# Kernel optimization log

Hardware: AMD Instinct MI355X
Metric: run time of the kernel (lower is better)

## Reference

```python
import jax, jax.numpy as jnp
import numpy as np

N_NODES = 100000
N_EDGES = 1600000
D_FEAT = 128
HIDDEN = 128
N_CLASSES = 10
NUM_GRAPHS = 64


def setup_inputs() -> dict:
    key = jax.random.key(0)
    ks = jax.random.split(key, 12)
    x = jax.random.normal(ks[0], (N_NODES, D_FEAT), dtype=jnp.float32)
    edge_index = jax.random.randint(ks[1], (2, N_EDGES), 0, N_NODES, dtype=jnp.int32)
    batch = jnp.sort(jax.random.randint(ks[2], (N_NODES,), 0, NUM_GRAPHS, dtype=jnp.int32))
    s = 1.0 / np.sqrt(HIDDEN)
    def lin(k, out_d, in_d):
        return jax.random.uniform(k, (out_d, in_d), jnp.float32, -s, s)
    return {
        "x": x,
        "edge_index": edge_index,
        "batch": batch,
        "W1l": lin(ks[3], HIDDEN, D_FEAT), "b1": jnp.zeros((HIDDEN,), jnp.float32),
        "W1r": lin(ks[4], HIDDEN, D_FEAT),
        "W2l": lin(ks[5], HIDDEN, HIDDEN), "b2": jnp.zeros((HIDDEN,), jnp.float32),
        "W2r": lin(ks[6], HIDDEN, HIDDEN),
        "W3l": lin(ks[7], HIDDEN, HIDDEN), "b3": jnp.zeros((HIDDEN,), jnp.float32),
        "W3r": lin(ks[8], HIDDEN, HIDDEN),
        "Wout": lin(ks[9], N_CLASSES, HIDDEN), "bout": jnp.zeros((N_CLASSES,), jnp.float32),
    }


def reference(x, edge_index, batch, W1l, b1, W1r, W2l, b2, W2r, W3l, b3, W3r, Wout, bout):
    src, dst = edge_index[0], edge_index[1]
    n = x.shape[0]

    def sage(h, Wl, b, Wr):
        # sum-aggregate neighbor features: scatter-add x[src] into dst rows
        agg = jax.ops.segment_sum(h[src], dst, num_segments=n)  # [N, d]
        return agg @ Wl.T + b + h @ Wr.T

    h = jax.nn.relu(sage(x, W1l, b1, W1r))
    h = jax.nn.relu(sage(h, W2l, b2, W2r))
    h = sage(h, W3l, b3, W3r)
    pooled = jax.ops.segment_sum(h, batch, num_segments=NUM_GRAPHS)  # [G, hidden]
    # dropout is identity in eval mode
    return pooled @ Wout.T + bout
```

## Files before the change

kernel.cpp:

```cpp
#include <hip/hip_runtime.h>
#include <hip/hip_bf16.h>

#define N_NODES  100000
#define N_EDGES  1600000
#define D_FEAT   128
#define HIDDEN   128
#define N_CLASSES 10
#define NUM_GRAPHS 64

#define NBUCK 250
#define NPB   400
#define BCAP  7168
#define GT    64
#define NPAD  100096
#define NTILES (NPAD / GT)

typedef __bf16 bf16x8 __attribute__((ext_vector_type(8)));
typedef float  f32x4  __attribute__((ext_vector_type(4)));

static __device__ __forceinline__ unsigned short f2bf(float f) {
    __bf16 b = (__bf16)f;
    return __builtin_bit_cast(unsigned short, b);
}

__global__ void conv_w6_kernel(const float* __restrict__ W0, const float* __restrict__ W1,
                               const float* __restrict__ W2, const float* __restrict__ W3,
                               const float* __restrict__ W4, const float* __restrict__ W5,
                               __bf16* __restrict__ out) {
    const float* Ws[6] = {W0, W1, W2, W3, W4, W5};
    int m = blockIdx.x >> 6;
    int i = (blockIdx.x & 63) * 256 + threadIdx.x;
    out[m * (HIDDEN * D_FEAT) + i] = (__bf16)Ws[m][i];
}

__global__ __launch_bounds__(256) void xconv_kernel(const float* __restrict__ x,
                                                    __bf16* __restrict__ out) {
    int i = blockIdx.x * 256 + threadIdx.x;
    bf16x8 o;
    if (i < N_NODES * 128 / 8) {
        float4 v0 = ((const float4*)x)[i * 2];
        float4 v1 = ((const float4*)x)[i * 2 + 1];
        o[0] = (__bf16)v0.x; o[1] = (__bf16)v0.y; o[2] = (__bf16)v0.z; o[3] = (__bf16)v0.w;
        o[4] = (__bf16)v1.x; o[5] = (__bf16)v1.y; o[6] = (__bf16)v1.z; o[7] = (__bf16)v1.w;
    } else {
        #pragma unroll
        for (int k = 0; k < 8; k++) o[k] = (__bf16)0.f;
    }
    if (i < NPAD * 128 / 8) ((bf16x8*)out)[i] = o;
}

__global__ __launch_bounds__(256) void bucket_scatter_kernel(const int* __restrict__ ei,
                                                             int* __restrict__ gcur,
                                                             int* __restrict__ bkt) {
    __shared__ int h[NBUCK];
    __shared__ int lb[NBUCK];
    int t = threadIdx.x;
    const int CH = N_EDGES / 256;
    for (int i = t; i < NBUCK; i += 256) h[i] = 0;
    __syncthreads();
    int e0 = blockIdx.x * CH;
    for (int e = e0 + t; e < e0 + CH; e += 256) {
        int d = ei[N_EDGES + e];
        atomicAdd(&h[d / NPB], 1);
    }
    __syncthreads();
    for (int i = t; i < NBUCK; i += 256) {
        lb[i] = atomicAdd(&gcur[i], h[i]);
        h[i] = 0;
    }
    __syncthreads();
    for (int e = e0 + t; e < e0 + CH; e += 256) {
        int s = ei[e];
        int d = ei[N_EDGES + e];
        int bb = d / NPB;
        int pos = lb[bb] + atomicAdd(&h[bb], 1);
        if (pos < BCAP) bkt[(size_t)bb * BCAP + pos] = ((d - bb * NPB) << 17) | s;
    }
}

__global__ __launch_bounds__(256) void bucket_csr_kernel(const int* __restrict__ bkt,
                                                         const int* __restrict__ gcur,
                                                         int2* __restrict__ rpse,
                                                         int* __restrict__ csr_src) {
    const int b = blockIdx.x;
    const int n0 = b * NPB;
    const int base = b * BCAP;
    int m = gcur[b]; if (m > BCAP) m = BCAP;
    __shared__ int cnt[NPB];
    __shared__ int part[128];
    __shared__ int excl[NPB];
    int t = threadIdx.x;
    for (int i = t; i < NPB; i += 256) cnt[i] = 0;
    __syncthreads();
    for (int e = t; e < m; e += 256) {
        int p = bkt[base + e];
        atomicAdd(&cnt[p >> 17], 1);
    }
    __syncthreads();
    int gs = 0;
    if (t < 100) { gs = cnt[4 * t] + cnt[4 * t + 1] + cnt[4 * t + 2] + cnt[4 * t + 3]; part[t] = gs; }
    else if (t < 128) part[t] = 0;
    __syncthreads();
    for (int off = 1; off < 128; off <<= 1) {
        int x = 0;
        if (t < 128 && t >= off) x = part[t - off];
        __syncthreads();
        if (t < 128) part[t] += x;
        __syncthreads();
    }
    if (t < 100) part[t] -= gs;
    __syncthreads();
    for (int i = t; i < NPB; i += 256) {
        int g = i >> 2;
        int e0 = part[g];
        for (int j = g * 4; j < i; j++) e0 += cnt[j];
        excl[i] = e0;
    }
    __syncthreads();
    for (int i = t; i < NPB; i += 256) {
        rpse[n0 + i] = make_int2(base + excl[i], base + excl[i] + cnt[i]);
    }
    __syncthreads();
    for (int i = t; i < NPB; i += 256) cnt[i] = excl[i];
    __syncthreads();
    for (int e = t; e < m; e += 256) {
        int p = bkt[base + e];
        int pos = base + atomicAdd(&cnt[p >> 17], 1);
        csr_src[pos] = p & 0x1FFFF;
    }
}

__global__ __launch_bounds__(256) void gather_kernel(
    const __bf16* __restrict__ h, const int2* __restrict__ rpse,
    const int* __restrict__ csr_src, __bf16* __restrict__ agg, int N)
{
    int nid = blockIdx.x * 16 + (threadIdx.x >> 4);
    if (nid >= N) return;
    int f8 = threadIdx.x & 15;
    int2 se = rpse[nid];

    float a[8] = {0.f, 0.f, 0.f, 0.f, 0.f, 0.f, 0.f, 0.f};

    int j = se.x;
    for (; j + 3 < se.y; j += 4) {
        int s0 = csr_src[j];
        int s1 = csr_src[j + 1];
        int s2 = csr_src[j + 2];
        int s3 = csr_src[j + 3];
        bf16x8 u0 = ((const bf16x8*)h)[(size_t)s0 * 16 + f8];
        bf16x8 u1 = ((const bf16x8*)h)[(size_t)s1 * 16 + f8];
        bf16x8 u2 = ((const bf16x8*)h)[(size_t)s2 * 16 + f8];
        bf16x8 u3 = ((const bf16x8*)h)[(size_t)s3 * 16 + f8];
        #pragma unroll
        for (int i = 0; i < 8; i++)
            a[i] += ((float)u0[i] + (float)u1[i]) + ((float)u2[i] + (float)u3[i]);
    }
    for (; j < se.y; j++) {
        int s0 = csr_src[j];
        bf16x8 u0 = ((const bf16x8*)h)[(size_t)s0 * 16 + f8];
        #pragma unroll
        for (int i = 0; i < 8; i++) a[i] += (float)u0[i];
    }
    bf16x8 o;
    #pragma unroll
    for (int i = 0; i < 8; i++) o[i] = (__bf16)a[i];
    ((bf16x8*)agg)[(size_t)nid * 16 + f8] = o;
}

template<bool RELU, bool POOL>
__global__ __launch_bounds__(256) void gemm_kernel(
    const __bf16* __restrict__ hA,
    const __bf16* __restrict__ hG,
    const __bf16* __restrict__ Wl, const __bf16* __restrict__ Wr,
    const float* __restrict__ bias,
    __bf16* __restrict__ outp, int M,
    const int* __restrict__ batch, float* __restrict__ pooled)
{
    const int tid  = threadIdx.x;
    const int wave = tid >> 6;
    const int lane = tid & 63;
    const int kq = lane >> 4;
    const int ln = lane & 15;
    const int node_base = blockIdx.x * GT;
    const int f_base = wave * 32;

    bf16x8 wfragL[2][4], wfragR[2][4];
    #pragma unroll
    for (int t = 0; t < 2; t++) {
        int wrow = f_base + t * 16 + ln;
        #pragma unroll
        for (int kc = 0; kc < 4; kc++) {
            int k0 = kc * 32 + kq * 8;
            wfragL[t][kc] = *(const bf16x8*)(Wl + wrow * 128 + k0);
            wfragR[t][kc] = *(const bf16x8*)(Wr + wrow * 128 + k0);
        }
    }
    float4 bias4[2];
    bias4[0] = *(const float4*)(bias + f_base + kq * 4);
    bias4[1] = *(const float4*)(bias + f_base + 16 + kq * 4);

    #pragma unroll 1
    for (int tau = 0; tau < GT / 16; tau++) {
        const int node = node_base + tau * 16 + ln;
        const size_t rowoff = (size_t)node * 128;
        bf16x8 gfrag[4], afrag[4];
        #pragma unroll
        for (int kc = 0; kc < 4; kc++) {
            gfrag[kc] = *(const bf16x8*)(hG + rowoff + kc * 32 + kq * 8);
            afrag[kc] = *(const bf16x8*)(hA + rowoff + kc * 32 + kq * 8);
        }

        f32x4 acc[2] = {(f32x4)(0.f), (f32x4)(0.f)};
        #pragma unroll
        for (int kc = 0; kc < 4; kc++) {
            #pragma unroll
            for (int t = 0; t < 2; t++) {
                acc[t] = __builtin_amdgcn_mfma_f32_16x16x32_bf16(wfragL[t][kc], gfrag[kc], acc[t], 0, 0, 0);
                acc[t] = __builtin_amdgcn_mfma_f32_16x16x32_bf16(wfragR[t][kc], afrag[kc], acc[t], 0, 0, 0);
            }
        }

        if (!POOL) {
            if (node < M) {
                #pragma unroll
                for (int t = 0; t < 2; t++) {
                    int fc = f_base + t * 16 + kq * 4;
                    float v0 = acc[t][0] + bias4[t].x;
                    float v1 = acc[t][1] + bias4[t].y;
                    float v2 = acc[t][2] + bias4[t].z;
                    float v3 = acc[t][3] + bias4[t].w;
                    if (RELU) {
                        v0 = fmaxf(v0, 0.f); v1 = fmaxf(v1, 0.f);
                        v2 = fmaxf(v2, 0.f); v3 = fmaxf(v3, 0.f);
                    }
                    ushort4 o;
                    o.x = f2bf(v0); o.y = f2bf(v1); o.z = f2bf(v2); o.w = f2bf(v3);
                    *(ushort4*)(outp + rowoff + fc) = o;
                }
            }
        } else {
            const int n0 = node_base + tau * 16;
            const bool uni = (n0 + 15 < M) && (batch[n0] == batch[n0 + 15]);
            #pragma unroll
            for (int t = 0; t < 2; t++) {
                int fc = f_base + t * 16 + kq * 4;
                float v0 = acc[t][0] + bias4[t].x;
                float v1 = acc[t][1] + bias4[t].y;
                float v2 = acc[t][2] + bias4[t].z;
                float v3 = acc[t][3] + bias4[t].w;
                if (uni) {
                    #pragma unroll
                    for (int m = 1; m < 16; m <<= 1) {
                        v0 += __shfl_xor(v0, m);
                        v1 += __shfl_xor(v1, m);
                        v2 += __shfl_xor(v2, m);
                        v3 += __shfl_xor(v3, m);
                    }
                    if (ln == 0) {
                        float* p = &pooled[(size_t)batch[n0] * HIDDEN + fc];
                        unsafeAtomicAdd(p + 0, v0);
                        unsafeAtomicAdd(p + 1, v1);
                        unsafeAtomicAdd(p + 2, v2);
                        unsafeAtomicAdd(p + 3, v3);
                    }
                } else if (node < M) {
                    float* p = &pooled[(size_t)batch[node] * HIDDEN + fc];
                    unsafeAtomicAdd(p + 0, v0);
                    unsafeAtomicAdd(p + 1, v1);
                    unsafeAtomicAdd(p + 2, v2);
                    unsafeAtomicAdd(p + 3, v3);
                }
            }
        }
    }
}

__global__ void final_gemm_kernel(
    const float* __restrict__ pooled, const float* __restrict__ Wout,
    const float* __restrict__ bout, float* __restrict__ out)
{
    int idx = blockIdx.x * 64 + threadIdx.x;
    if (idx < NUM_GRAPHS * N_CLASSES) {
        int g = idx / N_CLASSES;
        int c = idx % N_CLASSES;
        float acc = bout[c];
        for (int k = 0; k < HIDDEN; k++)
            acc += pooled[g * HIDDEN + k] * Wout[c * HIDDEN + k];
        out[idx] = acc;
    }
}

extern "C" void kernel_launch(void* const* d_in, const int* in_sizes, int n_in,
                              void* d_out, int out_size, void* d_ws, size_t ws_size,
                              hipStream_t stream) {
    const float* x     = (const float*)d_in[0];
    const int*   ei    = (const int*)d_in[1];
    const int*   batch = (const int*)d_in[2];
    const float* W1l = (const float*)d_in[3];
    const float* b1  = (const float*)d_in[4];
    const float* W1r = (const float*)d_in[5];
    const float* W2l = (const float*)d_in[6];
    const float* b2  = (const float*)d_in[7];
    const float* W2r = (const float*)d_in[8];
    const float* W3l = (const float*)d_in[9];
    const float* b3  = (const float*)d_in[10];
    const float* W3r = (const float*)d_in[11];
    const float* Wout = (const float*)d_in[12];
    const float* bout = (const float*)d_in[13];
    float* out = (float*)d_out;

    char* ws = (char*)d_ws;
    size_t off = 0;
    const size_t NB = (size_t)NPAD * 128 * sizeof(__bf16);
    __bf16* B0    = (__bf16*)(ws + off); off += NB;
    __bf16* B1    = (__bf16*)(ws + off); off += NB;
    __bf16* B2    = (__bf16*)(ws + off); off += NB;
    float* pooled = (float*)(ws + off);  off += (size_t)NUM_GRAPHS * HIDDEN * sizeof(float);
    __bf16* wbf   = (__bf16*)(ws + off); off += 6 * (size_t)HIDDEN * D_FEAT * sizeof(__bf16);
    int2* rpse    = (int2*)(ws + off);   off += (size_t)N_NODES * sizeof(int2);
    int* csr_src  = (int*)(ws + off);    off += (size_t)NBUCK * BCAP * sizeof(int);
    int* bkt      = (int*)(ws + off);    off += (size_t)NBUCK * BCAP * sizeof(int);
    int* gcur     = (int*)(ws + off);    off += (NBUCK + 8) * sizeof(int);

    const int WSZ = HIDDEN * D_FEAT;

    conv_w6_kernel<<<6 * 64, 256, 0, stream>>>(W1l, W1r, W2l, W2r, W3l, W3r, wbf);
    xconv_kernel<<<NPAD * 128 / (256 * 8), 256, 0, stream>>>(x, B0);

    hipMemsetAsync(gcur, 0, NBUCK * sizeof(int), stream);
    hipMemsetAsync(pooled, 0, (size_t)NUM_GRAPHS * HIDDEN * sizeof(float), stream);
    bucket_scatter_kernel<<<256, 256, 0, stream>>>(ei, gcur, bkt);
    bucket_csr_kernel<<<NBUCK, 256, 0, stream>>>(bkt, gcur, rpse, csr_src);

    const int gath_grid = (N_NODES + 15) / 16;

    gather_kernel<<<gath_grid, 256, 0, stream>>>(B0, rpse, csr_src, B1, N_NODES);
    gemm_kernel<true, false><<<NTILES, 256, 0, stream>>>(
        B0, B1, wbf + 0 * WSZ, wbf + 1 * WSZ, b1, B2, N_NODES, nullptr, nullptr);

    gather_kernel<<<gath_grid, 256, 0, stream>>>(B2, rpse, csr_src, B1, N_NODES);
    gemm_kernel<true, false><<<NTILES, 256, 0, stream>>>(
        B2, B1, wbf + 2 * WSZ, wbf + 3 * WSZ, b2, B0, N_NODES, nullptr, nullptr);

    gather_kernel<<<gath_grid, 256, 0, stream>>>(B0, rpse, csr_src, B1, N_NODES);
    gemm_kernel<false, true><<<NTILES, 256, 0, stream>>>(
        B0, B1, wbf + 4 * WSZ, wbf + 5 * WSZ, b3, nullptr, N_NODES, batch, pooled);

    final_gemm_kernel<<<10, 64, 0, stream>>>(pooled, Wout, bout, out);
}
```

Before: 507.5 us.

## Sort CSR neighbor lists and stage GEMM input tiles into LDS asynchronously

Adds a per-node insertion-sort pass over each node's CSR source list (up to 48 entries) so gathers visit source rows in ascending order, aiming at better cache locality. The GEMM kernel now bulk-loads its 64-row input tiles of both operands into swizzled LDS with global_load_lds before computing, instead of per-lane global fragment loads. The sort adds an extra kernel with heavy LDS use and thread divergence. The ReLU added in the pooled branch only runs in the non-ReLU instantiation's dead path.

```diff
diff --git a/kernel.cpp b/kernel.cpp
--- a/kernel.cpp
+++ b/kernel.cpp
@@ -14,6 +14,7 @@
 #define GT    64
 #define NPAD  100096
 #define NTILES (NPAD / GT)
+#define SORT_CAP 48
 
 typedef __bf16 bf16x8 __attribute__((ext_vector_type(8)));
 typedef float  f32x4  __attribute__((ext_vector_type(4)));
@@ -21,6 +22,12 @@
 static __device__ __forceinline__ unsigned short f2bf(float f) {
     __bf16 b = (__bf16)f;
     return __builtin_bit_cast(unsigned short, b);
+}
+
+static __device__ __forceinline__ void async_copy16(void* lds, const void* g) {
+    __builtin_amdgcn_global_load_lds(
+        (const __attribute__((address_space(1))) void*)g,
+        (__attribute__((address_space(3))) void*)lds, 16, 0, 0);
 }
 
 __global__ void conv_w6_kernel(const float* __restrict__ W0, const float* __restrict__ W1,
@@ -130,6 +137,26 @@
     }
 }
 
+__global__ __launch_bounds__(256) void sort_csr_kernel(const int2* __restrict__ rpse,
+                                                       int* __restrict__ csr_src, int N) {
+    __shared__ int buf[SORT_CAP][256];
+    int nid = blockIdx.x * 256 + threadIdx.x;
+    if (nid >= N) return;
+    int t = threadIdx.x;
+    int2 se = rpse[nid];
+    int deg = se.y - se.x;
+    if (deg <= 1) return;
+    if (deg > SORT_CAP) deg = SORT_CAP;
+    for (int j = 0; j < deg; j++) buf[j][t] = csr_src[se.x + j];
+    for (int i = 1; i < deg; i++) {
+        int key = buf[i][t];
+        int j = i - 1;
+        while (j >= 0 && buf[j][t] > key) { buf[j + 1][t] = buf[j][t]; j--; }
+        buf[j + 1][t] = key;
+    }
+    for (int j = 0; j < deg; j++) csr_src[se.x + j] = buf[j][t];
+}
+
 __global__ __launch_bounds__(256) void gather_kernel(
     const __bf16* __restrict__ h, const int2* __restrict__ rpse,
     const int* __restrict__ csr_src, __bf16* __restrict__ agg, int N)
@@ -168,7 +195,7 @@
 }
 
 template<bool RELU, bool POOL>
-__global__ __launch_bounds__(256) void gemm_kernel(
+__global__ __launch_bounds__(256) void fused_gemm_kernel(
     const __bf16* __restrict__ hA,
     const __bf16* __restrict__ hG,
     const __bf16* __restrict__ Wl, const __bf16* __restrict__ Wr,
@@ -176,6 +203,8 @@
     __bf16* __restrict__ outp, int M,
     const int* __restrict__ batch, float* __restrict__ pooled)
 {
+    __shared__ __bf16 lds[2][GT * 128];
+
     const int tid  = threadIdx.x;
     const int wave = tid >> 6;
     const int lane = tid & 63;
@@ -184,6 +213,19 @@
     const int node_base = blockIdx.x * GT;
     const int f_base = wave * 32;
 
+    {
+        const __bf16* gsrc = hG + (size_t)node_base * 128;
+        const __bf16* asrc = hA + (size_t)node_base * 128;
+        #pragma unroll
+        for (int i = 0; i < 4; i++) {
+            int u = i * 256 + tid;
+            int row = u >> 4;
+            int sc = (u & 15) ^ (row & 15);
+            async_copy16(&lds[0][u * 8], gsrc + row * 128 + sc * 8);
+            async_copy16(&lds[1][u * 8], asrc + row * 128 + sc * 8);
+        }
+    }
+
     bf16x8 wfragL[2][4], wfragR[2][4];
     #pragma unroll
     for (int t = 0; t < 2; t++) {
@@ -199,15 +241,17 @@
     bias4[0] = *(const float4*)(bias + f_base + kq * 4);
     bias4[1] = *(const float4*)(bias + f_base + 16 + kq * 4);
 
-    #pragma unroll 1
+    __syncthreads();
+
+    #pragma unroll 2
     for (int tau = 0; tau < GT / 16; tau++) {
-        const int node = node_base + tau * 16 + ln;
-        const size_t rowoff = (size_t)node * 128;
+        int r = tau * 16 + ln;
         bf16x8 gfrag[4], afrag[4];
         #pragma unroll
         for (int kc = 0; kc < 4; kc++) {
-            gfrag[kc] = *(const bf16x8*)(hG + rowoff + kc * 32 + kq * 8);
-            afrag[kc] = *(const bf16x8*)(hA + rowoff + kc * 32 + kq * 8);
+            int c = (4 * kc + kq) ^ ln;
+            gfrag[kc] = *(const bf16x8*)&lds[0][r * 128 + c * 8];
+            afrag[kc] = *(const bf16x8*)&lds[1][r * 128 + c * 8];
         }
 
         f32x4 acc[2] = {(f32x4)(0.f), (f32x4)(0.f)};
@@ -220,8 +264,10 @@
             }
         }
 
+        const int node = node_base + tau * 16 + ln;
         if (!POOL) {
             if (node < M) {
+                size_t rowoff = (size_t)node * 128;
                 #pragma unroll
                 for (int t = 0; t < 2; t++) {
                     int fc = f_base + t * 16 + kq * 4;
@@ -248,6 +294,10 @@
                 float v1 = acc[t][1] + bias4[t].y;
                 float v2 = acc[t][2] + bias4[t].z;
                 float v3 = acc[t][3] + bias4[t].w;
+                if (RELU) {
+                    v0 = fmaxf(v0, 0.f); v1 = fmaxf(v1, 0.f);
+                    v2 = fmaxf(v2, 0.f); v3 = fmaxf(v3, 0.f);
+                }
                 if (uni) {
                     #pragma unroll
                     for (int m = 1; m < 16; m <<= 1) {
@@ -331,19 +381,20 @@
     hipMemsetAsync(pooled, 0, (size_t)NUM_GRAPHS * HIDDEN * sizeof(float), stream);
     bucket_scatter_kernel<<<256, 256, 0, stream>>>(ei, gcur, bkt);
     bucket_csr_kernel<<<NBUCK, 256, 0, stream>>>(bkt, gcur, rpse, csr_src);
+    sort_csr_kernel<<<(N_NODES + 255) / 256, 256, 0, stream>>>(rpse, csr_src, N_NODES);
 
     const int gath_grid = (N_NODES + 15) / 16;
 
     gather_kernel<<<gath_grid, 256, 0, stream>>>(B0, rpse, csr_src, B1, N_NODES);
-    gemm_kernel<true, false><<<NTILES, 256, 0, stream>>>(
+    fused_gemm_kernel<true, false><<<NTILES, 256, 0, stream>>>(
         B0, B1, wbf + 0 * WSZ, wbf + 1 * WSZ, b1, B2, N_NODES, nullptr, nullptr);
 
     gather_kernel<<<gath_grid, 256, 0, stream>>>(B2, rpse, csr_src, B1, N_NODES);
-    gemm_kernel<true, false><<<NTILES, 256, 0, stream>>>(
+    fused_gemm_kernel<true, false><<<NTILES, 256, 0, stream>>>(
         B2, B1, wbf + 2 * WSZ, wbf + 3 * WSZ, b2, B0, N_NODES, nullptr, nullptr);
 
     gather_kernel<<<gath_grid, 256, 0, stream>>>(B0, rpse, csr_src, B1, N_NODES);
-    gemm_kernel<false, true><<<NTILES, 256, 0, stream>>>(
+    fused_gemm_kernel<false, true><<<NTILES, 256, 0, stream>>>(
         B0, B1, wbf + 4 * WSZ, wbf + 5 * WSZ, b3, nullptr, N_NODES, batch, pooled);
 
     final_gemm_kernel<<<10, 64, 0, stream>>>(pooled, Wout, bout, out);
```

Measured after the change: 498.6 us. About the same (-1.8%).
